# Performance work log

Hardware: AMD Instinct MI355X
Metric: run time of the kernel (lower is better)

## Reference

```python
import jax, jax.numpy as jnp
import numpy as np

C = 512
H_HEADS = 8
CTX_D = 768
GEO_D = 512
FFN_D = 4 * C
EPS = 1e-5


def _layernorm(x, g, b):
    mu = jnp.mean(x, axis=-1, keepdims=True)
    var = jnp.mean((x - mu) ** 2, axis=-1, keepdims=True)
    return (x - mu) * jax.lax.rsqrt(var + EPS) * g + b


def _cross_attn(x, ctx, Wq, Wk, Wv, Wo, bo, h):
    # x: (B, N, C), ctx: (B, S, Dctx)
    b, n, _ = x.shape
    s = ctx.shape[1]
    inner = Wq.shape[1]
    d = inner // h
    q = (x @ Wq).reshape(b, n, h, d)
    k = (ctx @ Wk).reshape(b, s, h, d)
    v = (ctx @ Wv).reshape(b, s, h, d)
    sim = jnp.einsum('bihd,bjhd->bhij', q, k) * (d ** -0.5)
    attn = jax.nn.softmax(sim, axis=-1)
    out = jnp.einsum('bhij,bjhd->bihd', attn, v).reshape(b, n, inner)
    return out @ Wo + bo


def setup_inputs() -> dict:
    key = jax.random.key(0)
    ks = jax.random.split(key, 24)
    std = lambda fan_in: 1.0 / np.sqrt(fan_in)
    inp = {
        'x': jax.random.normal(ks[0], (4, C, 64, 64), jnp.float32),
        'context': jax.random.normal(ks[1], (4, 77, CTX_D), jnp.float32),
        'geometry_tokens': jax.random.normal(ks[2], (4, 256, GEO_D), jnp.float32),
        # layernorm params (norm1..norm4)
        'g1': jnp.ones((C,)), 'b1': jnp.zeros((C,)),
        'g2': jnp.ones((C,)), 'b2': jnp.zeros((C,)),
        'g3': jnp.ones((C,)), 'b3': jnp.zeros((C,)),
        'g4': jnp.ones((C,)), 'b4': jnp.zeros((C,)),
        # cross-attention (context) weights
        'cWq': jax.random.normal(ks[3], (C, C)) * std(C),
        'cWk': jax.random.normal(ks[4], (CTX_D, C)) * std(CTX_D),
        'cWv': jax.random.normal(ks[5], (CTX_D, C)) * std(CTX_D),
        'cWo': jax.random.normal(ks[6], (C, C)) * std(C),
        'cbo': jnp.zeros((C,)),
        # geometry-attention weights
        'gWq': jax.random.normal(ks[7], (C, C)) * std(C),
        'gWk': jax.random.normal(ks[8], (GEO_D, C)) * std(GEO_D),
        'gWv': jax.random.normal(ks[9], (GEO_D, C)) * std(GEO_D),
        'gWo': jax.random.normal(ks[10], (C, C)) * std(C),
        'gbo': jnp.zeros((C,)),
        # FFN weights
        'W1': jax.random.normal(ks[11], (C, FFN_D)) * std(C),
        'bf1': jnp.zeros((FFN_D,)),
        'W2': jax.random.normal(ks[12], (FFN_D, C)) * std(FFN_D),
        'bf2': jnp.zeros((C,)),
    }
    return inp


def reference(x, context, geometry_tokens,
              g1, b1, g2, b2, g3, b3, g4, b4,
              cWq, cWk, cWv, cWo, cbo,
              gWq, gWk, gWv, gWo, gbo,
              W1, bf1, W2, bf2):
    b, c, h, w = x.shape
    t = x.reshape(b, c, h * w).transpose(0, 2, 1)  # (B, N, C)
    # self_attn is called with context=None -> identity, so this is t + norm1(t)
    t = t + _layernorm(t, g1, b1)
    t = t + _cross_attn(_layernorm(t, g2, b2), context, cWq, cWk, cWv, cWo, cbo, H_HEADS)
    t = t + _cross_attn(_layernorm(t, g3, b3), geometry_tokens, gWq, gWk, gWv, gWo, gbo, H_HEADS)
    hdn = jax.nn.gelu(_layernorm(t, g4, b4) @ W1 + bf1, approximate=False)
    t = t + hdn @ W2 + bf2
    return t.transpose(0, 2, 1).reshape(b, c, h, w)
```

## Files before the change

kernel.cpp:

```cpp
#include <hip/hip_runtime.h>
#include <hip/hip_bf16.h>

using bf16 = __hip_bfloat16;
typedef __attribute__((ext_vector_type(8))) short short8;
typedef __attribute__((ext_vector_type(4))) short short4v;
typedef __attribute__((ext_vector_type(4))) float floatx4;

#define DEVFN __device__ __forceinline__

DEVFN float bf2f(bf16 v) { return __bfloat162float(v); }
DEVFN bf16 f2bf(float v) { return __float2bfloat16(v); }
DEVFN float us2f(unsigned short u) {
    union { unsigned int i; float f; } c; c.i = ((unsigned int)u) << 16; return c.f;
}
DEVFN unsigned short f2bfbits(float v) {
    union { bf16 h; unsigned short u; } c; c.h = f2bf(v); return c.u;
}
DEVFN float loadF(const void* p, size_t i, int isf) {
    return isf ? ((const float*)p)[i] : us2f(((const unsigned short*)p)[i]);
}
DEVFN void gl_lds16(const bf16* g, short* l) {
    __builtin_amdgcn_global_load_lds(
        (const __attribute__((address_space(1))) unsigned int*)g,
        (__attribute__((address_space(3))) unsigned int*)l, 16, 0, 0);
}
DEVFN float fast_gelu(float v) {
    float u = v * (0.7978845608028654f + 0.0356774081f * v * v);
    float e = __expf(2.f * u);
    float th = 1.f - 2.f / (e + 1.f);
    return 0.5f * v * (1.f + th);
}

__global__ __launch_bounds__(256) void detect_kernel(const void* x, int* flag)
{
    __shared__ int any;
    if (threadIdx.x == 0) any = 0;
    __syncthreads();
    const unsigned short* p = (const unsigned short*)x;
    int hit = 0;
    for (int i = threadIdx.x; i < 8192; i += 256) {
        if ((p[i] & 0x7F80u) == 0x7F80u) hit = 1;
    }
    if (hit) any = 1;
    __syncthreads();
    if (threadIdx.x == 0) flag[0] = any;
}

__global__ __launch_bounds__(256) void convert_kernel(
    const void* __restrict__ src, bf16* __restrict__ dst, const int* __restrict__ flag, int n)
{
    int isf = *flag;
    int i = blockIdx.x * 256 + threadIdx.x;
    if (i < n) dst[i] = f2bf(loadF(src, i, isf));
}

struct SegTab {
    const void* src[12];
    int off[12];
    int cnt[12];
};
__global__ __launch_bounds__(256) void param_convert_kernel(
    SegTab tab, bf16* __restrict__ dst, const int* __restrict__ flag)
{
    int isf = *flag;
    int s = blockIdx.x;
    const void* src = tab.src[s];
    int off = tab.off[s], cnt = tab.cnt[s];
    for (int i = threadIdx.x; i < cnt; i += 256)
        dst[off + i] = f2bf(loadF(src, i, isf));
}

__global__ __launch_bounds__(256) void ln_in_kernel(
    const void* __restrict__ x, float* __restrict__ t,
    const bf16* __restrict__ g, const bf16* __restrict__ bta,
    const int* __restrict__ flag, int NN)
{
    __shared__ float tile[16][516];
    int isf = *flag;
    int b = blockIdx.y;
    int n0 = blockIdx.x * 16;
    int tid = threadIdx.x;
    int nx = tid & 15, cy = tid >> 4;
#pragma unroll
    for (int p = 0; p < 32; p++) {
        int c = p * 16 + cy;
        tile[nx][c] = loadF(x, ((size_t)b * 512 + c) * NN + n0 + nx, isf);
    }
    __syncthreads();
    int w = tid >> 6, lane = tid & 63;
    for (int rr = 0; rr < 4; rr++) {
        int r = w * 4 + rr;
        float4 v0 = *(const float4*)&tile[r][lane * 8];
        float4 v1 = *(const float4*)&tile[r][lane * 8 + 4];
        float vals[8] = {v0.x, v0.y, v0.z, v0.w, v1.x, v1.y, v1.z, v1.w};
        float s = 0.f;
#pragma unroll
        for (int i = 0; i < 8; i++) s += vals[i];
#pragma unroll
        for (int off = 32; off; off >>= 1) s += __shfl_xor(s, off, 64);
        float mu = s * (1.f / 512.f);
        float sq = 0.f;
#pragma unroll
        for (int i = 0; i < 8; i++) { float d = vals[i] - mu; sq += d * d; }
#pragma unroll
        for (int off = 32; off; off >>= 1) sq += __shfl_xor(sq, off, 64);
        float rs = rsqrtf(sq * (1.f / 512.f) + 1e-5f);
        float out[8];
#pragma unroll
        for (int i = 0; i < 8; i++) {
            int c = lane * 8 + i;
            out[i] = vals[i] + (vals[i] - mu) * rs * bf2f(g[c]) + bf2f(bta[c]);
        }
        float* tp = t + ((size_t)b * NN + n0 + r) * 512 + lane * 8;
        *(float4*)tp = make_float4(out[0], out[1], out[2], out[3]);
        *(float4*)(tp + 4) = make_float4(out[4], out[5], out[6], out[7]);
    }
}

__global__ __launch_bounds__(256) void transpose_out_kernel(
    const float* __restrict__ t, void* __restrict__ o, const int* __restrict__ flag,
    int C, int NN)
{
    __shared__ float tile[32][33];
    int isf = *flag;
    int b = blockIdx.z;
    int n0 = blockIdx.x * 32, c0 = blockIdx.y * 32;
    int tx = threadIdx.x, ty = threadIdx.y;
#pragma unroll
    for (int i = 0; i < 4; i++)
        tile[ty + i * 8][tx] = t[((size_t)b * NN + n0 + ty + i * 8) * C + c0 + tx];
    __syncthreads();
#pragma unroll
    for (int i = 0; i < 4; i++) {
        size_t oi = ((size_t)b * C + c0 + ty + i * 8) * NN + n0 + tx;
        float val = tile[tx][ty + i * 8];
        if (isf) ((float*)o)[oi] = val;
        else ((bf16*)o)[oi] = f2bf(val);
    }
}

__global__ __launch_bounds__(256) void transpose_w_kernel(
    const void* __restrict__ Wm, bf16* __restrict__ WT, const int* __restrict__ flag,
    int K, int Nc)
{
    __shared__ float tile[32][33];
    int isf = *flag;
    int n0 = blockIdx.x * 32, k0 = blockIdx.y * 32;
    int tx = threadIdx.x, ty = threadIdx.y;
#pragma unroll
    for (int i = 0; i < 4; i++)
        tile[ty + i * 8][tx] = loadF(Wm, (size_t)(k0 + ty + i * 8) * Nc + n0 + tx, isf);
    __syncthreads();
#pragma unroll
    for (int i = 0; i < 4; i++)
        WT[(size_t)(n0 + ty + i * 8) * K + k0 + tx] = f2bf(tile[tx][ty + i * 8]);
}

__global__ __launch_bounds__(256) void ln_kernel(
    const float* __restrict__ t, const bf16* __restrict__ g, const bf16* __restrict__ bta,
    bf16* __restrict__ outp, int Mrows)
{
    int w = threadIdx.x >> 6, lane = threadIdx.x & 63;
    int row = blockIdx.x * 4 + w;
    if (row >= Mrows) return;
    const float* xr = t + (size_t)row * 512;
    float4 v0 = *(const float4*)(xr + lane * 8);
    float4 v1 = *(const float4*)(xr + lane * 8 + 4);
    float vals[8] = {v0.x, v0.y, v0.z, v0.w, v1.x, v1.y, v1.z, v1.w};
    float s = 0.f;
#pragma unroll
    for (int i = 0; i < 8; i++) s += vals[i];
#pragma unroll
    for (int off = 32; off; off >>= 1) s += __shfl_xor(s, off, 64);
    float mu = s * (1.f / 512.f);
    float sq = 0.f;
#pragma unroll
    for (int i = 0; i < 8; i++) { float d = vals[i] - mu; sq += d * d; }
#pragma unroll
    for (int off = 32; off; off >>= 1) sq += __shfl_xor(sq, off, 64);
    float rs = rsqrtf(sq * (1.f / 512.f) + 1e-5f);
#pragma unroll
    for (int i = 0; i < 8; i++) {
        int c = lane * 8 + i;
        float y = (vals[i] - mu) * rs * bf2f(g[c]) + bf2f(bta[c]);
        outp[(size_t)row * 512 + c] = f2bf(y);
    }
}

template <int MODE>
__global__ __launch_bounds__(256) void gemm64(
    const bf16* __restrict__ A, const bf16* __restrict__ WT,
    const bf16* __restrict__ bias, void* __restrict__ outp,
    int M, int K, int Nc)
{
    __shared__ short As[64 * 32];
    __shared__ short Bs[64 * 32];
    const int tid = threadIdx.x;
    const int m0 = blockIdx.y * 64;
    const int n0 = blockIdx.x * 64;
    const int w = tid >> 6;
    const int lane = tid & 63;
    const int lm = lane & 15;
    const int lq = lane >> 4;

    floatx4 acc[4];
#pragma unroll
    for (int nb = 0; nb < 4; nb++) acc[nb] = (floatx4){0.f, 0.f, 0.f, 0.f};

    const int srow = tid >> 2;
    const int scol = (tid & 3) << 3;
    const int agrow = m0 + srow;
    const bool aok = agrow < M;
    const bf16* Aptr = A + (size_t)agrow * K + scol;
    const bf16* Bptr = WT + (size_t)(n0 + srow) * K + scol;

    for (int k0 = 0; k0 < K; k0 += 32) {
        __syncthreads();
        int4 av = make_int4(0, 0, 0, 0);
        if (aok) av = *(const int4*)(Aptr + k0);
        *(int4*)(&As[srow * 32 + scol]) = av;
        *(int4*)(&Bs[srow * 32 + scol]) = *(const int4*)(Bptr + k0);
        __syncthreads();
        short8 a = *(const short8*)(&As[(w * 16 + lm) * 32 + lq * 8]);
#pragma unroll
        for (int nb = 0; nb < 4; nb++) {
            short8 b = *(const short8*)(&Bs[(nb * 16 + lm) * 32 + lq * 8]);
            acc[nb] = __builtin_amdgcn_mfma_f32_16x16x32_bf16(a, b, acc[nb], 0, 0, 0);
        }
    }

#pragma unroll
    for (int nb = 0; nb < 4; nb++) {
        int col = n0 + nb * 16 + lm;
        float bv = bias ? bf2f(bias[col]) : 0.f;
#pragma unroll
        for (int r = 0; r < 4; r++) {
            int row = m0 + w * 16 + lq * 4 + r;
            if (row < M) {
                float v = acc[nb][r] + bv;
                if (MODE == 1) v = fast_gelu(v);
                if (MODE == 2) {
                    ((float*)outp)[(size_t)row * Nc + col] += v;
                } else {
                    ((bf16*)outp)[(size_t)row * Nc + col] = f2bf(v);
                }
            }
        }
    }
}

#define MFMA_PAIR(RB, A00, A01, A10, A11)                                              \
    _Pragma("unroll")                                                                   \
    for (int cb = 0; cb < CB; cb++) {                                                   \
        acc[cb][RB]     = __builtin_amdgcn_mfma_f32_16x16x32_bf16(bf0[cb], A00, acc[cb][RB], 0, 0, 0);     \
        acc[cb][RB]     = __builtin_amdgcn_mfma_f32_16x16x32_bf16(bf1[cb], A01, acc[cb][RB], 0, 0, 0);     \
        acc[cb][RB + 1] = __builtin_amdgcn_mfma_f32_16x16x32_bf16(bf0[cb], A10, acc[cb][RB + 1], 0, 0, 0); \
        acc[cb][RB + 1] = __builtin_amdgcn_mfma_f32_16x16x32_bf16(bf1[cb], A11, acc[cb][RB + 1], 0, 0, 0); \
    }

template <int MODE, int CB>
__global__ __launch_bounds__(512, 2) void gemm8p(
    const bf16* __restrict__ A, const bf16* __restrict__ WT,
    const bf16* __restrict__ bias, void* __restrict__ outp,
    int K, int Nc)
{
    constexpr int BN = CB * 64;
    constexpr int ABUF = 256 * 64;
    constexpr int BBUF = BN * 64;
    __shared__ short As[2 * ABUF];
    __shared__ short Bs[2 * BBUF];

    const int tid = threadIdx.x;
    const int gx = gridDim.x;
    int g = blockIdx.y * gx + blockIdx.x;
    const int cpx = (gx * gridDim.y) >> 3;
    g = (g & 7) * cpx + (g >> 3);
    const int m0 = (g / gx) * 256;
    const int n0 = (g % gx) * BN;

    const int w = tid >> 6, lane = tid & 63;
    const int lm = lane & 15, lq = lane >> 4;
    const int wm = w >> 2, wn = w & 3;

    floatx4 acc[CB][8];
#pragma unroll
    for (int cb = 0; cb < CB; cb++)
#pragma unroll
        for (int rb = 0; rb < 8; rb++) acc[cb][rb] = (floatx4){0.f, 0.f, 0.f, 0.f};

    const int rbaseA = (tid >> 3) + ((tid >= 256) ? 96 : 0);
    const int chk = (((tid & 7) ^ ((tid >> 3) & 7)) << 3);
    const bf16* pA = A + (size_t)(m0 + rbaseA) * K + chk;
    const int rbaseB = ((tid >> 7) << (CB == 4 ? 6 : 5)) + ((tid >> 3) & 15);
    const bf16* pB = WT + (size_t)(n0 + rbaseB) * K + chk;
    const int wbA = w * 512 + ((w >= 4) ? 6144 : 0);
    const int wbB = (CB == 4) ? ((w >> 1) * 4096 + (w & 1) * 512)
                              : ((w >> 1) * 2048 + (w & 1) * 512);
    const size_t K32 = (size_t)K * 32;
    const size_t K16 = (size_t)K * 16;

    const int arow = (wm * 128 + lm) * 64;
    const int brow = (wn * CB * 16 + lm) * 64;
    const int sl0 = ((lq ^ (lm & 7)) << 3);
    const int sl1 = (((4 + lq) ^ (lm & 7)) << 3);

    const int nt = K >> 6;

#pragma unroll
    for (int q = 0; q < 4; q++) gl_lds16(pA + (size_t)q * K32, As + q * 2048 + wbA);
    if constexpr (CB == 4) {
        gl_lds16(pB,           Bs + wbB);
        gl_lds16(pB + K16,     Bs + 1024 + wbB);
        gl_lds16(pB + 2 * K16, Bs + 2048 + wbB);
        gl_lds16(pB + 3 * K16, Bs + 3072 + wbB);
    } else {
        gl_lds16(pB,       Bs + wbB);
        gl_lds16(pB + K16, Bs + 1024 + wbB);
    }
    {
        const bf16* qA = pA + 64;
        const bf16* qB = pB + 64;
        if constexpr (CB == 4) {
            gl_lds16(qB,           Bs + BBUF + wbB);
            gl_lds16(qB + K16,     Bs + BBUF + 1024 + wbB);
            gl_lds16(qB + 2 * K16, Bs + BBUF + 2048 + wbB);
            gl_lds16(qB + 3 * K16, Bs + BBUF + 3072 + wbB);
            gl_lds16(qA,           As + ABUF + wbA);
            gl_lds16(qA + K32,     As + ABUF + 2048 + wbA);
            asm volatile("s_waitcnt vmcnt(6)\n\ts_barrier" ::: "memory");
        } else {
            gl_lds16(qB,           Bs + BBUF + wbB);
            gl_lds16(qB + K16, Bs + BBUF + 1024 + wbB);
            gl_lds16(qA,           As + ABUF + wbA);
            gl_lds16(qA + K32,     As + ABUF + 2048 + wbA);
            gl_lds16(qA + 2 * K32, As + ABUF + 4096 + wbA);
            asm volatile("s_waitcnt vmcnt(5)\n\ts_barrier" ::: "memory");
        }
    }

    for (int s = 0; s < nt; ++s) {
        const int cu = s & 1;
        const short* cA = As + cu * ABUF;
        const short* cB = Bs + cu * BBUF;
        short* oA = As + (cu ^ 1) * ABUF;
        short* sA = As + cu * ABUF;
        short* sB = Bs + cu * BBUF;
        const bf16* pA1 = pA + (s + 1) * 64;
        const bf16* pA2 = pA + (s + 2) * 64;
        const bf16* pB2 = pB + (s + 2) * 64;
        short8 bf0[CB], bf1[CB], x0, x1, y0, y1;

#pragma unroll
        for (int cb = 0; cb < CB; cb++) {
            bf0[cb] = *(const short8*)&cB[brow + cb * 1024 + sl0];
            bf1[cb] = *(const short8*)&cB[brow + cb * 1024 + sl1];
        }
        x0 = *(const short8*)&cA[arow + sl0];
        x1 = *(const short8*)&cA[arow + sl1];
        y0 = *(const short8*)&cA[arow + 1024 + sl0];
        y1 = *(const short8*)&cA[arow + 1024 + sl1];
        if (s + 1 < nt) {
            if constexpr (CB == 4) {
                gl_lds16(pA1 + 2 * K32, oA + 2 * 2048 + wbA);
                gl_lds16(pA1 + 3 * K32, oA + 3 * 2048 + wbA);
            } else {
                gl_lds16(pA1 + 3 * K32, oA + 3 * 2048 + wbA);
            }
        }
        asm volatile("s_barrier" ::: "memory");
        __builtin_amdgcn_s_setprio(1);
        MFMA_PAIR(0, x0, x1, y0, y1)
        __builtin_amdgcn_s_setprio(0);
        asm volatile("s_waitcnt lgkmcnt(0)\n\ts_barrier" ::: "memory");

        x0 = *(const short8*)&cA[arow + 2 * 1024 + sl0];
        x1 = *(const short8*)&cA[arow + 2 * 1024 + sl1];
        y0 = *(const short8*)&cA[arow + 3 * 1024 + sl0];
        y1 = *(const short8*)&cA[arow + 3 * 1024 + sl1];
        if (s + 2 < nt) {
            gl_lds16(pB2,       sB + wbB);
            gl_lds16(pB2 + K16, sB + 1024 + wbB);
        }
        asm volatile("s_barrier" ::: "memory");
        __builtin_amdgcn_s_setprio(1);
        MFMA_PAIR(2, x0, x1, y0, y1)
        __builtin_amdgcn_s_setprio(0);
        asm volatile("s_waitcnt lgkmcnt(0)\n\ts_barrier" ::: "memory");

        x0 = *(const short8*)&cA[arow + 4 * 1024 + sl0];
        x1 = *(const short8*)&cA[arow + 4 * 1024 + sl1];
        y0 = *(const short8*)&cA[arow + 5 * 1024 + sl0];
        y1 = *(const short8*)&cA[arow + 5 * 1024 + sl1];
        if (s + 2 < nt) {
            if constexpr (CB == 4) {
                gl_lds16(pB2 + 2 * K16, sB + 2048 + wbB);
                gl_lds16(pB2 + 3 * K16, sB + 3072 + wbB);
            } else {
                gl_lds16(pA2, sA + wbA);
            }
        }
        asm volatile("s_barrier" ::: "memory");
        __builtin_amdgcn_s_setprio(1);
        MFMA_PAIR(4, x0, x1, y0, y1)
        __builtin_amdgcn_s_setprio(0);
        asm volatile("s_waitcnt lgkmcnt(0)\n\ts_barrier" ::: "memory");

        x0 = *(const short8*)&cA[arow + 6 * 1024 + sl0];
        x1 = *(const short8*)&cA[arow + 6 * 1024 + sl1];
        y0 = *(const short8*)&cA[arow + 7 * 1024 + sl0];
        y1 = *(const short8*)&cA[arow + 7 * 1024 + sl1];
        if (s + 2 < nt) {
            if constexpr (CB == 4) {
                gl_lds16(pA2,       sA + wbA);
                gl_lds16(pA2 + K32, sA + 2048 + wbA);
            } else {
                gl_lds16(pA2 + K32,     sA + 2048 + wbA);
                gl_lds16(pA2 + 2 * K32, sA + 4096 + wbA);
            }
        }
        asm volatile("s_barrier" ::: "memory");
        __builtin_amdgcn_s_setprio(1);
        MFMA_PAIR(6, x0, x1, y0, y1)
        __builtin_amdgcn_s_setprio(0);
        if (s <= nt - 3) {
            if constexpr (CB == 4)
                asm volatile("s_waitcnt vmcnt(6) lgkmcnt(0)\n\ts_barrier" ::: "memory");
            else
                asm volatile("s_waitcnt vmcnt(5) lgkmcnt(0)\n\ts_barrier" ::: "memory");
        } else if (s == nt - 2) {
            asm volatile("s_waitcnt vmcnt(0) lgkmcnt(0)\n\ts_barrier" ::: "memory");
        } else {
            asm volatile("s_waitcnt lgkmcnt(0)\n\ts_barrier" ::: "memory");
        }
    }
    __syncthreads();

    float4 bias4[CB];
#pragma unroll
    for (int cb = 0; cb < CB; cb++) {
        if (bias) {
            const bf16* bp = bias + n0 + wn * (CB * 16) + cb * 16 + lq * 4;
            bias4[cb] = make_float4(bf2f(bp[0]), bf2f(bp[1]), bf2f(bp[2]), bf2f(bp[3]));
        } else {
            bias4[cb] = make_float4(0.f, 0.f, 0.f, 0.f);
        }
    }

    if constexpr (MODE == 2) {
        float* po = (float*)outp;
#pragma unroll
        for (int rb = 0; rb < 8; rb++) {
            size_t m = m0 + wm * 128 + rb * 16 + lm;
#pragma unroll
            for (int cb = 0; cb < CB; cb++) {
                float* p = po + m * Nc + n0 + wn * (CB * 16) + cb * 16 + lq * 4;
                float4 f = *(float4*)p;
                f.x += acc[cb][rb][0] + bias4[cb].x;
                f.y += acc[cb][rb][1] + bias4[cb].y;
                f.z += acc[cb][rb][2] + bias4[cb].z;
                f.w += acc[cb][rb][3] + bias4[cb].w;
                *(float4*)p = f;
            }
        }
    } else if constexpr (CB == 2) {
        unsigned short* op = (unsigned short*)outp;
#pragma unroll
        for (int rb = 0; rb < 8; rb++) {
            size_t m = m0 + wm * 128 + rb * 16 + lm;
#pragma unroll
            for (int cb = 0; cb < 2; cb++) {
                short4v pk;
#pragma unroll
                for (int r = 0; r < 4; r++) {
                    float vv = acc[cb][rb][r] + ((const float*)&bias4[cb])[r];
                    if (MODE == 1) vv = fast_gelu(vv);
                    pk[r] = (short)f2bfbits(vv);
                }
                *(short4v*)(op + m * Nc + n0 + wn * 32 + cb * 16 + lq * 4) = pk;
            }
        }
    } else {
        unsigned short* stgb = (unsigned short*)&As[w * 1024];
        unsigned short* op = (unsigned short*)outp;
#pragma unroll
        for (int rb = 0; rb < 8; rb++) {
#pragma unroll
            for (int cb = 0; cb < 4; cb++) {
                short4v pk;
#pragma unroll
                for (int r = 0; r < 4; r++) {
                    float vv = acc[cb][rb][r] + ((const float*)&bias4[cb])[r];
                    if (MODE == 1) vv = fast_gelu(vv);
                    pk[r] = (short)f2bfbits(vv);
                }
                int chunk = (cb * 2 + (lq >> 1)) ^ (lm & 7);
                *(short4v*)(&stgb[lm * 64 + chunk * 8 + (lq & 1) * 4]) = pk;
            }
#pragma unroll
            for (int p = 0; p < 2; p++) {
                int row = p * 8 + (lane >> 3);
                int chunk = lane & 7;
                short8 ov = *(const short8*)(&stgb[row * 64 + ((chunk ^ (row & 7)) * 8)]);
                size_t m = m0 + wm * 128 + rb * 16 + row;
                *(short8*)(op + m * Nc + n0 + wn * 64 + chunk * 8) = ov;
            }
        }
    }
}

template <int SPAD, int SVALID>
__global__ __launch_bounds__(256) void attn_mfma_kernel(
    const bf16* __restrict__ q, const bf16* __restrict__ k, const bf16* __restrict__ v,
    bf16* __restrict__ o, int N)
{
    constexpr int MB = SPAD / 16;
    constexpr int KS = SPAD / 32;
    __shared__ unsigned short lds[SPAD * 64 + 64 * SPAD];
    unsigned short* Ks = lds;
    unsigned short* Vt = lds + SPAD * 64;
    unsigned short* Pw = lds;

    const int tid = threadIdx.x;
    const int b = blockIdx.x >> 3;
    const int h = blockIdx.x & 7;
    const int n0 = blockIdx.y * 64;
    const int w = tid >> 6, lane = tid & 63;
    const int lm = lane & 15, lq = lane >> 4;

    const unsigned short* kp = (const unsigned short*)k;
    const unsigned short* vp = (const unsigned short*)v;
    for (int idx = tid * 8; idx < SPAD * 64; idx += 2048) {
        int s = idx >> 6, d0 = idx & 63;
        short8 kv = {0, 0, 0, 0, 0, 0, 0, 0};
        short8 vv = {0, 0, 0, 0, 0, 0, 0, 0};
        if (s < SVALID) {
            size_t gb = ((size_t)(b * SVALID + s)) * 512 + h * 64 + d0;
            kv = *(const short8*)(kp + gb);
            vv = *(const short8*)(vp + gb);
        }
        int kc = (d0 >> 3) ^ (s & 7);
        *(short8*)(&Ks[s * 64 + kc * 8]) = kv;
        const unsigned short* vvp = (const unsigned short*)&vv;
#pragma unroll
        for (int i = 0; i < 8; i++) {
            int d = d0 + i;
            int sc = (s >> 3) ^ (d & 7);
            Vt[d * SPAD + sc * 8 + (s & 7)] = vvp[i];
        }
    }

    const int q0 = n0 + w * 16;
    const unsigned short* qp = (const unsigned short*)q;
    size_t qbase = ((size_t)(b * N + q0 + lm)) * 512 + h * 64 + lq * 8;
    short8 qf0 = *(const short8*)(qp + qbase);
    short8 qf1 = *(const short8*)(qp + qbase + 32);
    __syncthreads();

    floatx4 sacc[MB];
#pragma unroll
    for (int mb = 0; mb < MB; mb++) sacc[mb] = (floatx4){0.f, 0.f, 0.f, 0.f};
#pragma unroll
    for (int mb = 0; mb < MB; mb++) {
        int srow = mb * 16 + lm;
        short8 a0 = *(const short8*)(&Ks[srow * 64 + ((lq ^ (lm & 7)) * 8)]);
        short8 a1 = *(const short8*)(&Ks[srow * 64 + (((4 + lq) ^ (lm & 7)) * 8)]);
        sacc[mb] = __builtin_amdgcn_mfma_f32_16x16x32_bf16(a0, qf0, sacc[mb], 0, 0, 0);
        sacc[mb] = __builtin_amdgcn_mfma_f32_16x16x32_bf16(a1, qf1, sacc[mb], 0, 0, 0);
    }

    float mx = -1e30f;
#pragma unroll
    for (int mb = 0; mb < MB; mb++)
#pragma unroll
        for (int r = 0; r < 4; r++) {
            int s = mb * 16 + lq * 4 + r;
            if (s < SVALID) mx = fmaxf(mx, sacc[mb][r]);
        }
    mx = fmaxf(mx, __shfl_xor(mx, 16, 64));
    mx = fmaxf(mx, __shfl_xor(mx, 32, 64));
    mx *= 0.125f;
    float sum = 0.f;
#pragma unroll
    for (int mb = 0; mb < MB; mb++)
#pragma unroll
        for (int r = 0; r < 4; r++) {
            int s = mb * 16 + lq * 4 + r;
            float e = (s < SVALID) ? __expf(sacc[mb][r] * 0.125f - mx) : 0.f;
            sacc[mb][r] = e;
            sum += e;
        }
    sum += __shfl_xor(sum, 16, 64);
    sum += __shfl_xor(sum, 32, 64);
    float inv = 1.f / sum;

    __syncthreads();

    unsigned short* Pme = Pw + w * 16 * SPAD;
#pragma unroll
    for (int mb = 0; mb < MB; mb++) {
        short4v pk;
        pk[0] = (short)f2bfbits(sacc[mb][0] * inv);
        pk[1] = (short)f2bfbits(sacc[mb][1] * inv);
        pk[2] = (short)f2bfbits(sacc[mb][2] * inv);
        pk[3] = (short)f2bfbits(sacc[mb][3] * inv);
        int chunk = (mb * 2 + (lq >> 1)) ^ (lm & 7);
        *(short4v*)(&Pme[lm * SPAD + chunk * 8 + (lq & 1) * 4]) = pk;
    }

    floatx4 oacc[4];
#pragma unroll
    for (int mb2 = 0; mb2 < 4; mb2++) oacc[mb2] = (floatx4){0.f, 0.f, 0.f, 0.f};
    for (int ks = 0; ks < KS; ks++) {
        int sch = ((ks * 4 + lq) ^ (lm & 7)) * 8;
        short8 bfrag = *(const short8*)(&Pme[lm * SPAD + sch]);
#pragma unroll
        for (int mb2 = 0; mb2 < 4; mb2++) {
            int d = mb2 * 16 + lm;
            short8 afrag = *(const short8*)(&Vt[d * SPAD + sch]);
            oacc[mb2] = __builtin_amdgcn_mfma_f32_16x16x32_bf16(afrag, bfrag, oacc[mb2], 0, 0, 0);
        }
    }

#pragma unroll
    for (int mb2 = 0; mb2 < 4; mb2++) {
        short4v ok;
        ok[0] = (short)f2bfbits(oacc[mb2][0]);
        ok[1] = (short)f2bfbits(oacc[mb2][1]);
        ok[2] = (short)f2bfbits(oacc[mb2][2]);
        ok[3] = (short)f2bfbits(oacc[mb2][3]);
        int chunk = (mb2 * 2 + (lq >> 1)) ^ (lm & 7);
        *(short4v*)(&Pme[lm * 64 + chunk * 8 + (lq & 1) * 4]) = ok;
    }
    unsigned short* op = (unsigned short*)o;
#pragma unroll
    for (int p = 0; p < 2; p++) {
        int row = p * 8 + (lane >> 3);
        int chunk = lane & 7;
        short8 ov = *(const short8*)(&Pme[row * 64 + ((chunk ^ (row & 7)) * 8)]);
        *(short8*)(op + ((size_t)(b * N + n0 + w * 16 + row)) * 512 + h * 64 + chunk * 8) = ov;
    }
}

extern "C" void kernel_launch(void* const* d_in, const int* in_sizes, int n_in,
                              void* d_out, int out_size, void* d_ws, size_t ws_size,
                              hipStream_t stream)
{
    const void* x   = d_in[0];
    const void* ctx = d_in[1];
    const void* geo = d_in[2];
    const void* g1 = d_in[3];  const void* b1 = d_in[4];
    const void* g2 = d_in[5];  const void* b2 = d_in[6];
    const void* g3 = d_in[7];  const void* b3 = d_in[8];
    const void* g4 = d_in[9];  const void* b4 = d_in[10];
    const void* cWq = d_in[11]; const void* cWk = d_in[12];
    const void* cWv = d_in[13]; const void* cWo = d_in[14];
    const void* cbo = d_in[15];
    const void* gWq = d_in[16]; const void* gWk = d_in[17];
    const void* gWv = d_in[18]; const void* gWo = d_in[19];
    const void* gbo = d_in[20];
    const void* W1 = d_in[21];  const void* bf1 = d_in[22];
    const void* W2 = d_in[23];  const void* bf2 = d_in[24];

    const int B = 4, C = 512, NN = 4096;
    const int M = B * NN;

    char* ws = (char*)d_ws;
    size_t off = 0;
    auto alloc = [&](size_t bytes) -> void* {
        void* p = ws + off; off += (bytes + 255) & ~(size_t)255; return p;
    };
    int*   flag = (int*)alloc(256);
    float* t  = (float*)alloc((size_t)M * C * 4);
    bf16* u   = (bf16*)alloc((size_t)M * C * 2);
    bf16* qb  = (bf16*)alloc((size_t)M * C * 2);
    bf16* kb  = (bf16*)alloc((size_t)B * 256 * C * 2);
    bf16* vb  = (bf16*)alloc((size_t)B * 256 * C * 2);
    bf16* ctxb = (bf16*)alloc((size_t)B * 77 * 768 * 2);
    bf16* geob = (bf16*)alloc((size_t)B * 256 * 512 * 2);
    bf16* cWqT = (bf16*)alloc((size_t)512 * 512 * 2);
    bf16* cWkT = (bf16*)alloc((size_t)512 * 768 * 2);
    bf16* cWvT = (bf16*)alloc((size_t)512 * 768 * 2);
    bf16* cWoT = (bf16*)alloc((size_t)512 * 512 * 2);
    bf16* gWqT = (bf16*)alloc((size_t)512 * 512 * 2);
    bf16* gWkT = (bf16*)alloc((size_t)512 * 512 * 2);
    bf16* gWvT = (bf16*)alloc((size_t)512 * 512 * 2);
    bf16* gWoT = (bf16*)alloc((size_t)512 * 512 * 2);
    bf16* W1T  = (bf16*)alloc((size_t)2048 * 512 * 2);
    bf16* W2T  = (bf16*)alloc((size_t)512 * 2048 * 2);
    bf16* prm  = (bf16*)alloc((size_t)7680 * 2);
    bf16* ob = u;

    int chunk;
    bf16* hb;
    size_t rem = (ws_size > off) ? (ws_size - off) : 0;
    if (rem >= (size_t)16384 * 2048 * 2) { chunk = 16384; hb = (bf16*)alloc((size_t)16384 * 2048 * 2); }
    else if (rem >= (size_t)8192 * 2048 * 2) { chunk = 8192; hb = (bf16*)alloc((size_t)8192 * 2048 * 2); }
    else { chunk = 4096; hb = qb; }
    (void)in_sizes; (void)n_in; (void)out_size;

    bf16 *pg1 = prm, *pb1 = prm + 512, *pg2 = prm + 1024, *pb2 = prm + 1536;
    bf16 *pg3 = prm + 2048, *pb3 = prm + 2560, *pg4 = prm + 3072, *pb4 = prm + 3584;
    bf16 *pcbo = prm + 4096, *pgbo = prm + 4608, *pbf1 = prm + 5120, *pbf2 = prm + 7168;

    dim3 tb(32, 8);

    detect_kernel<<<1, 256, 0, stream>>>(x, flag);
    SegTab tab;
    const void* srcs[12] = {g1, b1, g2, b2, g3, b3, g4, b4, cbo, gbo, bf1, bf2};
    int offs[12] = {0, 512, 1024, 1536, 2048, 2560, 3072, 3584, 4096, 4608, 5120, 7168};
    int cnts[12] = {512, 512, 512, 512, 512, 512, 512, 512, 512, 512, 2048, 512};
    for (int i = 0; i < 12; i++) { tab.src[i] = srcs[i]; tab.off[i] = offs[i]; tab.cnt[i] = cnts[i]; }
    param_convert_kernel<<<12, 256, 0, stream>>>(tab, prm, flag);
    convert_kernel<<<(B * 77 * 768 + 255) / 256, 256, 0, stream>>>(ctx, ctxb, flag, B * 77 * 768);
    convert_kernel<<<(B * 256 * 512 + 255) / 256, 256, 0, stream>>>(geo, geob, flag, B * 256 * 512);

    ln_in_kernel<<<dim3(NN / 16, B), 256, 0, stream>>>(x, t, pg1, pb1, flag, NN);

    transpose_w_kernel<<<dim3(512 / 32, 512 / 32), tb, 0, stream>>>(cWq, cWqT, flag, 512, 512);
    transpose_w_kernel<<<dim3(512 / 32, 768 / 32), tb, 0, stream>>>(cWk, cWkT, flag, 768, 512);
    transpose_w_kernel<<<dim3(512 / 32, 768 / 32), tb, 0, stream>>>(cWv, cWvT, flag, 768, 512);
    transpose_w_kernel<<<dim3(512 / 32, 512 / 32), tb, 0, stream>>>(cWo, cWoT, flag, 512, 512);
    transpose_w_kernel<<<dim3(512 / 32, 512 / 32), tb, 0, stream>>>(gWq, gWqT, flag, 512, 512);
    transpose_w_kernel<<<dim3(512 / 32, 512 / 32), tb, 0, stream>>>(gWk, gWkT, flag, 512, 512);
    transpose_w_kernel<<<dim3(512 / 32, 512 / 32), tb, 0, stream>>>(gWv, gWvT, flag, 512, 512);
    transpose_w_kernel<<<dim3(512 / 32, 512 / 32), tb, 0, stream>>>(gWo, gWoT, flag, 512, 512);
    transpose_w_kernel<<<dim3(2048 / 32, 512 / 32), tb, 0, stream>>>(W1, W1T, flag, 512, 2048);
    transpose_w_kernel<<<dim3(512 / 32, 2048 / 32), tb, 0, stream>>>(W2, W2T, flag, 2048, 512);

    ln_kernel<<<M / 4, 256, 0, stream>>>(t, pg2, pb2, u, M);
    gemm8p<0, 2><<<dim3(4, M / 256), 512, 0, stream>>>(u, cWqT, nullptr, qb, 512, 512);
    gemm64<0><<<dim3(8, (308 + 63) / 64), 256, 0, stream>>>(ctxb, cWkT, nullptr, kb, 308, 768, 512);
    gemm64<0><<<dim3(8, (308 + 63) / 64), 256, 0, stream>>>(ctxb, cWvT, nullptr, vb, 308, 768, 512);
    attn_mfma_kernel<128, 77><<<dim3(B * 8, NN / 64), 256, 0, stream>>>(qb, kb, vb, ob, NN);
    gemm8p<2, 2><<<dim3(4, M / 256), 512, 0, stream>>>(ob, cWoT, pcbo, t, 512, 512);

    ln_kernel<<<M / 4, 256, 0, stream>>>(t, pg3, pb3, u, M);
    gemm8p<0, 2><<<dim3(4, M / 256), 512, 0, stream>>>(u, gWqT, nullptr, qb, 512, 512);
    gemm64<0><<<dim3(8, 1024 / 64), 256, 0, stream>>>(geob, gWkT, nullptr, kb, 1024, 512, 512);
    gemm64<0><<<dim3(8, 1024 / 64), 256, 0, stream>>>(geob, gWvT, nullptr, vb, 1024, 512, 512);
    attn_mfma_kernel<256, 256><<<dim3(B * 8, NN / 64), 256, 0, stream>>>(qb, kb, vb, ob, NN);
    gemm8p<2, 2><<<dim3(4, M / 256), 512, 0, stream>>>(ob, gWoT, pgbo, t, 512, 512);

    ln_kernel<<<M / 4, 256, 0, stream>>>(t, pg4, pb4, u, M);
    for (int mc = 0; mc < M / chunk; mc++) {
        bf16* uc = u + (size_t)mc * chunk * 512;
        float* tc = t + (size_t)mc * chunk * 512;
        gemm8p<1, 4><<<dim3(2048 / 256, chunk / 256), 512, 0, stream>>>(uc, W1T, pbf1, hb, 512, 2048);
        gemm8p<2, 2><<<dim3(512 / 128, chunk / 256), 512, 0, stream>>>(hb, W2T, pbf2, tc, 2048, 512);
    }

    transpose_out_kernel<<<dim3(NN / 32, C / 32, B), tb, 0, stream>>>(t, d_out, flag, C, NN);
}
```

Measured before the change: 516.7 us.

## Batch conversion, weight transpose and K/V GEMM launches; add nontemporal memory hints

Merges the parameter and context conversion kernels into one table-driven launch, the ten weight transposes into one launch, and each K/V projection pair into a single GEMM launch using blockIdx.z. This cuts kernel launch count and lets small kernels fill the GPU together. It also adds nontemporal loads and stores on the residual stream in LN, the residual-add GEMM epilogue, the GELU hidden output and the output transpose, to reduce cache pollution. Nontemporal hints can backfire if the data is reused soon, for example t read by the next LN.

```diff
diff --git a/kernel.cpp b/kernel.cpp
--- a/kernel.cpp
+++ b/kernel.cpp
@@ -46,28 +46,27 @@
     if (threadIdx.x == 0) flag[0] = any;
 }
 
-__global__ __launch_bounds__(256) void convert_kernel(
-    const void* __restrict__ src, bf16* __restrict__ dst, const int* __restrict__ flag, int n)
+struct CVTab {
+    const void* src[14];
+    bf16* dst[14];
+    int cnt[14];
+    int bstart[14];
+};
+__global__ __launch_bounds__(256) void convert_batch_kernel(
+    CVTab tab, const int* __restrict__ flag)
 {
     int isf = *flag;
-    int i = blockIdx.x * 256 + threadIdx.x;
-    if (i < n) dst[i] = f2bf(loadF(src, i, isf));
-}
-
-struct SegTab {
-    const void* src[12];
-    int off[12];
-    int cnt[12];
-};
-__global__ __launch_bounds__(256) void param_convert_kernel(
-    SegTab tab, bf16* __restrict__ dst, const int* __restrict__ flag)
-{
-    int isf = *flag;
-    int s = blockIdx.x;
+    int b = blockIdx.x;
+    int s = 0;
+#pragma unroll
+    for (int i = 1; i < 14; i++) if (b >= tab.bstart[i]) s = i;
     const void* src = tab.src[s];
-    int off = tab.off[s], cnt = tab.cnt[s];
-    for (int i = threadIdx.x; i < cnt; i += 256)
-        dst[off + i] = f2bf(loadF(src, i, isf));
+    bf16* dst = tab.dst[s];
+    int cnt = tab.cnt[s];
+    int base = (b - tab.bstart[s]) * 2048;
+    int lim = min(base + 2048, cnt);
+    for (int i = base + (int)threadIdx.x; i < lim; i += 256)
+        dst[i] = f2bf(loadF(src, i, isf));
 }
 
 __global__ __launch_bounds__(256) void ln_in_kernel(
@@ -128,7 +127,8 @@
     int tx = threadIdx.x, ty = threadIdx.y;
 #pragma unroll
     for (int i = 0; i < 4; i++)
-        tile[ty + i * 8][tx] = t[((size_t)b * NN + n0 + ty + i * 8) * C + c0 + tx];
+        tile[ty + i * 8][tx] = __builtin_nontemporal_load(
+            &t[((size_t)b * NN + n0 + ty + i * 8) * C + c0 + tx]);
     __syncthreads();
 #pragma unroll
     for (int i = 0; i < 4; i++) {
@@ -139,13 +139,28 @@
     }
 }
 
-__global__ __launch_bounds__(256) void transpose_w_kernel(
-    const void* __restrict__ Wm, bf16* __restrict__ WT, const int* __restrict__ flag,
-    int K, int Nc)
+struct TWTab {
+    const void* src[10];
+    bf16* dst[10];
+    int K[10];
+    int Nc[10];
+    int tstart[10];
+};
+__global__ __launch_bounds__(256) void transpose_w_batch(
+    TWTab tab, const int* __restrict__ flag)
 {
     __shared__ float tile[32][33];
     int isf = *flag;
-    int n0 = blockIdx.x * 32, k0 = blockIdx.y * 32;
+    int b = blockIdx.x;
+    int s = 0;
+#pragma unroll
+    for (int i = 1; i < 10; i++) if (b >= tab.tstart[i]) s = i;
+    const void* Wm = tab.src[s];
+    bf16* WT = tab.dst[s];
+    int K = tab.K[s], Nc = tab.Nc[s];
+    int lt = b - tab.tstart[s];
+    int ntx = Nc >> 5;
+    int n0 = (lt % ntx) * 32, k0 = (lt / ntx) * 32;
     int tx = threadIdx.x, ty = threadIdx.y;
 #pragma unroll
     for (int i = 0; i < 4; i++)
@@ -164,9 +179,9 @@
     int row = blockIdx.x * 4 + w;
     if (row >= Mrows) return;
     const float* xr = t + (size_t)row * 512;
-    float4 v0 = *(const float4*)(xr + lane * 8);
-    float4 v1 = *(const float4*)(xr + lane * 8 + 4);
-    float vals[8] = {v0.x, v0.y, v0.z, v0.w, v1.x, v1.y, v1.z, v1.w};
+    floatx4 v0 = __builtin_nontemporal_load((const floatx4*)(xr + lane * 8));
+    floatx4 v1 = __builtin_nontemporal_load((const floatx4*)(xr + lane * 8 + 4));
+    float vals[8] = {v0[0], v0[1], v0[2], v0[3], v1[0], v1[1], v1[2], v1[3]};
     float s = 0.f;
 #pragma unroll
     for (int i = 0; i < 8; i++) s += vals[i];
@@ -188,11 +203,14 @@
 }
 
 template <int MODE>
-__global__ __launch_bounds__(256) void gemm64(
-    const bf16* __restrict__ A, const bf16* __restrict__ WT,
-    const bf16* __restrict__ bias, void* __restrict__ outp,
+__global__ __launch_bounds__(256) void gemm64x2(
+    const bf16* __restrict__ A,
+    const bf16* __restrict__ WT0, const bf16* __restrict__ WT1,
+    bf16* __restrict__ o0, bf16* __restrict__ o1,
     int M, int K, int Nc)
 {
+    const bf16* WT = blockIdx.z ? WT1 : WT0;
+    bf16* outp = blockIdx.z ? o1 : o0;
     __shared__ short As[64 * 32];
     __shared__ short Bs[64 * 32];
     const int tid = threadIdx.x;
@@ -232,18 +250,13 @@
 #pragma unroll
     for (int nb = 0; nb < 4; nb++) {
         int col = n0 + nb * 16 + lm;
-        float bv = bias ? bf2f(bias[col]) : 0.f;
 #pragma unroll
         for (int r = 0; r < 4; r++) {
             int row = m0 + w * 16 + lq * 4 + r;
             if (row < M) {
-                float v = acc[nb][r] + bv;
+                float v = acc[nb][r];
                 if (MODE == 1) v = fast_gelu(v);
-                if (MODE == 2) {
-                    ((float*)outp)[(size_t)row * Nc + col] += v;
-                } else {
-                    ((bf16*)outp)[(size_t)row * Nc + col] = f2bf(v);
-                }
+                outp[(size_t)row * Nc + col] = f2bf(v);
             }
         }
     }
@@ -454,12 +467,12 @@
 #pragma unroll
             for (int cb = 0; cb < CB; cb++) {
                 float* p = po + m * Nc + n0 + wn * (CB * 16) + cb * 16 + lq * 4;
-                float4 f = *(float4*)p;
-                f.x += acc[cb][rb][0] + bias4[cb].x;
-                f.y += acc[cb][rb][1] + bias4[cb].y;
-                f.z += acc[cb][rb][2] + bias4[cb].z;
-                f.w += acc[cb][rb][3] + bias4[cb].w;
-                *(float4*)p = f;
+                floatx4 f = __builtin_nontemporal_load((const floatx4*)p);
+                f[0] += acc[cb][rb][0] + bias4[cb].x;
+                f[1] += acc[cb][rb][1] + bias4[cb].y;
+                f[2] += acc[cb][rb][2] + bias4[cb].z;
+                f[3] += acc[cb][rb][3] + bias4[cb].w;
+                __builtin_nontemporal_store(f, (floatx4*)p);
             }
         }
     } else if constexpr (CB == 2) {
@@ -502,7 +515,9 @@
                 int chunk = lane & 7;
                 short8 ov = *(const short8*)(&stgb[row * 64 + ((chunk ^ (row & 7)) * 8)]);
                 size_t m = m0 + wm * 128 + rb * 16 + row;
-                *(short8*)(op + m * Nc + n0 + wn * 64 + chunk * 8) = ov;
+                short8* dst = (short8*)(op + m * Nc + n0 + wn * 64 + chunk * 8);
+                if (MODE == 1) __builtin_nontemporal_store(ov, dst);
+                else *dst = ov;
             }
         }
     }
@@ -705,39 +720,50 @@
     dim3 tb(32, 8);
 
     detect_kernel<<<1, 256, 0, stream>>>(x, flag);
-    SegTab tab;
-    const void* srcs[12] = {g1, b1, g2, b2, g3, b3, g4, b4, cbo, gbo, bf1, bf2};
-    int offs[12] = {0, 512, 1024, 1536, 2048, 2560, 3072, 3584, 4096, 4608, 5120, 7168};
-    int cnts[12] = {512, 512, 512, 512, 512, 512, 512, 512, 512, 512, 2048, 512};
-    for (int i = 0; i < 12; i++) { tab.src[i] = srcs[i]; tab.off[i] = offs[i]; tab.cnt[i] = cnts[i]; }
-    param_convert_kernel<<<12, 256, 0, stream>>>(tab, prm, flag);
-    convert_kernel<<<(B * 77 * 768 + 255) / 256, 256, 0, stream>>>(ctx, ctxb, flag, B * 77 * 768);
-    convert_kernel<<<(B * 256 * 512 + 255) / 256, 256, 0, stream>>>(geo, geob, flag, B * 256 * 512);
+
+    {
+        CVTab cv;
+        const void* csrc[14] = {g1, b1, g2, b2, g3, b3, g4, b4, cbo, gbo, bf1, bf2, ctx, geo};
+        bf16* cdst[14] = {prm, prm + 512, prm + 1024, prm + 1536, prm + 2048, prm + 2560,
+                          prm + 3072, prm + 3584, prm + 4096, prm + 4608, prm + 5120,
+                          prm + 7168, ctxb, geob};
+        int ccnt[14] = {512, 512, 512, 512, 512, 512, 512, 512, 512, 512, 2048, 512,
+                        B * 77 * 768, B * 256 * 512};
+        int bacc = 0;
+        for (int i = 0; i < 14; i++) {
+            cv.src[i] = csrc[i]; cv.dst[i] = cdst[i]; cv.cnt[i] = ccnt[i];
+            cv.bstart[i] = bacc;
+            bacc += (ccnt[i] + 2047) / 2048;
+        }
+        convert_batch_kernel<<<bacc, 256, 0, stream>>>(cv, flag);
+    }
 
     ln_in_kernel<<<dim3(NN / 16, B), 256, 0, stream>>>(x, t, pg1, pb1, flag, NN);
 
-    transpose_w_kernel<<<dim3(512 / 32, 512 / 32), tb, 0, stream>>>(cWq, cWqT, flag, 512, 512);
-    transpose_w_kernel<<<dim3(512 / 32, 768 / 32), tb, 0, stream>>>(cWk, cWkT, flag, 768, 512);
-    transpose_w_kernel<<<dim3(512 / 32, 768 / 32), tb, 0, stream>>>(cWv, cWvT, flag, 768, 512);
-    transpose_w_kernel<<<dim3(512 / 32, 512 / 32), tb, 0, stream>>>(cWo, cWoT, flag, 512, 512);
-    transpose_w_kernel<<<dim3(512 / 32, 512 / 32), tb, 0, stream>>>(gWq, gWqT, flag, 512, 512);
-    transpose_w_kernel<<<dim3(512 / 32, 512 / 32), tb, 0, stream>>>(gWk, gWkT, flag, 512, 512);
-    transpose_w_kernel<<<dim3(512 / 32, 512 / 32), tb, 0, stream>>>(gWv, gWvT, flag, 512, 512);
-    transpose_w_kernel<<<dim3(512 / 32, 512 / 32), tb, 0, stream>>>(gWo, gWoT, flag, 512, 512);
-    transpose_w_kernel<<<dim3(2048 / 32, 512 / 32), tb, 0, stream>>>(W1, W1T, flag, 512, 2048);
-    transpose_w_kernel<<<dim3(512 / 32, 2048 / 32), tb, 0, stream>>>(W2, W2T, flag, 2048, 512);
+    {
+        TWTab tw;
+        const void* wsrc[10] = {cWq, cWk, cWv, cWo, gWq, gWk, gWv, gWo, W1, W2};
+        bf16* wdst[10] = {cWqT, cWkT, cWvT, cWoT, gWqT, gWkT, gWvT, gWoT, W1T, W2T};
+        int wK[10]  = {512, 768, 768, 512, 512, 512, 512, 512, 512, 2048};
+        int wNc[10] = {512, 512, 512, 512, 512, 512, 512, 512, 2048, 512};
+        int tacc = 0;
+        for (int i = 0; i < 10; i++) {
+            tw.src[i] = wsrc[i]; tw.dst[i] = wdst[i]; tw.K[i] = wK[i]; tw.Nc[i] = wNc[i];
+            tw.tstart[i] = tacc;
+            tacc += (wNc[i] / 32) * (wK[i] / 32);
+        }
+        transpose_w_batch<<<tacc, tb, 0, stream>>>(tw, flag);
+    }
 
     ln_kernel<<<M / 4, 256, 0, stream>>>(t, pg2, pb2, u, M);
     gemm8p<0, 2><<<dim3(4, M / 256), 512, 0, stream>>>(u, cWqT, nullptr, qb, 512, 512);
-    gemm64<0><<<dim3(8, (308 + 63) / 64), 256, 0, stream>>>(ctxb, cWkT, nullptr, kb, 308, 768, 512);
-    gemm64<0><<<dim3(8, (308 + 63) / 64), 256, 0, stream>>>(ctxb, cWvT, nullptr, vb, 308, 768, 512);
+    gemm64x2<0><<<dim3(8, (308 + 63) / 64, 2), 256, 0, stream>>>(ctxb, cWkT, cWvT, kb, vb, 308, 768, 512);
     attn_mfma_kernel<128, 77><<<dim3(B * 8, NN / 64), 256, 0, stream>>>(qb, kb, vb, ob, NN);
     gemm8p<2, 2><<<dim3(4, M / 256), 512, 0, stream>>>(ob, cWoT, pcbo, t, 512, 512);
 
     ln_kernel<<<M / 4, 256, 0, stream>>>(t, pg3, pb3, u, M);
     gemm8p<0, 2><<<dim3(4, M / 256), 512, 0, stream>>>(u, gWqT, nullptr, qb, 512, 512);
-    gemm64<0><<<dim3(8, 1024 / 64), 256, 0, stream>>>(geob, gWkT, nullptr, kb, 1024, 512, 512);
-    gemm64<0><<<dim3(8, 1024 / 64), 256, 0, stream>>>(geob, gWvT, nullptr, vb, 1024, 512, 512);
+    gemm64x2<0><<<dim3(8, 1024 / 64, 2), 256, 0, stream>>>(geob, gWkT, gWvT, kb, vb, 1024, 512, 512);
     attn_mfma_kernel<256, 256><<<dim3(B * 8, NN / 64), 256, 0, stream>>>(qb, kb, vb, ob, NN);
     gemm8p<2, 2><<<dim3(4, M / 256), 512, 0, stream>>>(ob, gWoT, pgbo, t, 512, 512);
 
```

New measurement: 529.1 us. 1.02x slower.
